# Optimization experiments

Measured on AMD Instinct MI355X. Metric: run time of the kernel, lower is better.

Reference implementation:

```python
import jax, jax.numpy as jnp
import numpy as np

N_NODES = 100000
N_EDGES = 640000
HIDDEN = 128
EPS = 1e-6


def setup_inputs() -> dict:
    key = jax.random.key(0)
    k_x, k_w, k_a, k_e = jax.random.split(key, 4)
    x = jax.random.normal(k_x, (N_NODES, HIDDEN), dtype=jnp.float32)
    W = jax.random.normal(k_w, (HIDDEN, HIDDEN), dtype=jnp.float32) / np.sqrt(HIDDEN)
    b = jnp.zeros((HIDDEN,), dtype=jnp.float32)
    att_w = jax.random.normal(k_a, (1, 2 * HIDDEN), dtype=jnp.float32) / np.sqrt(2 * HIDDEN)
    norm_w = jnp.ones((HIDDEN,), dtype=jnp.float32)
    norm_b = jnp.zeros((HIDDEN,), dtype=jnp.float32)
    e = jax.random.randint(k_e, (N_EDGES, 2), 0, N_NODES, dtype=jnp.int64)
    return {"x": x, "W": W, "b": b, "att_w": att_w, "norm_w": norm_w, "norm_b": norm_b, "e": e}


def reference(x, W, b, att_w, norm_w, norm_b, e):
    n_nodes = x.shape[0]
    src, dst = e[:, 0], e[:, 1]
    # Edge gather + shared linear on both endpoints: [E, D]
    m = x[src] @ W.T + b
    s = x[dst] @ W.T + b
    # Attention score per edge: leaky_relu(concat @ w^T), then exp -> [E, 1]
    a = jnp.exp(jax.nn.leaky_relu(jnp.concatenate((m, s), axis=1) @ att_w.T, negative_slope=0.2))
    # NOTE: faithful to the original: this weighted message sum is computed
    # but then overwritten (dead code in the source module).
    _unused = jax.ops.segment_sum(a * m, dst, num_segments=n_nodes)
    # Normalizer: sum of attention weights per destination node -> [N, 1]
    n = jax.ops.segment_sum(a, dst, num_segments=n_nodes)
    h = jax.nn.relu(x / jnp.where(n == 0.0, 1.0, n))
    # Residual + RMSNorm (per-row, with affine weight and bias, eps=1e-6)
    y = h + x
    inv_rms = jax.lax.rsqrt(jnp.mean(y * y, axis=-1, keepdims=True) + EPS)
    return norm_w * (y * inv_rms) + norm_b
```

## Files before the change

kernel.cpp:

```cpp
#include <hip/hip_runtime.h>

#define N_NODES 100000
#define N_EDGES 640000
#define HIDDEN  128
#define EPS     1e-6f

__global__ void precompute_uvc(const float* __restrict__ W,
                               const float* __restrict__ b,
                               const float* __restrict__ att_w,
                               float* __restrict__ u,
                               float* __restrict__ v,
                               float* __restrict__ c) {
    int k = threadIdx.x;
    float su = 0.f, sv = 0.f;
    for (int j = 0; j < HIDDEN; ++j) {
        float w = W[j * HIDDEN + k];
        su += att_w[j] * w;
        sv += att_w[HIDDEN + j] * w;
    }
    u[k] = su;
    v[k] = sv;
    if (k == 0) {
        float cc = 0.f;
        for (int j = 0; j < HIDDEN; ++j)
            cc += att_w[j] * b[j] + att_w[HIDDEN + j] * b[j];
        *c = cc;
    }
}

__global__ void node_dots(const float* __restrict__ x,
                          const float* __restrict__ u,
                          const float* __restrict__ v,
                          float* __restrict__ p,
                          float* __restrict__ q) {
    int node = (int)((blockIdx.x * (unsigned)blockDim.x + threadIdx.x) >> 6);
    int lane = threadIdx.x & 63;
    if (node >= N_NODES) return;

    float2 xv = ((const float2*)(x + (size_t)node * HIDDEN))[lane];
    float2 uv = ((const float2*)u)[lane];
    float2 vv = ((const float2*)v)[lane];

    float sp = xv.x * uv.x + xv.y * uv.y;
    float sq = xv.x * vv.x + xv.y * vv.y;
    #pragma unroll
    for (int off = 32; off > 0; off >>= 1) {
        sp += __shfl_down(sp, off);
        sq += __shfl_down(sq, off);
    }
    if (lane == 0) { p[node] = sp; q[node] = sq; }
}

__global__ void edge_kernel(const int* __restrict__ e,
                            const float* __restrict__ p,
                            const float* __restrict__ q,
                            const float* __restrict__ c,
                            float* __restrict__ n) {
    int eid = blockIdx.x * blockDim.x + threadIdx.x;
    if (eid >= N_EDGES) return;
    int src = e[2 * eid];
    int dst = e[2 * eid + 1];
    float score = p[src] + q[dst] + c[0];
    float lr = score > 0.f ? score : 0.2f * score;
    atomicAdd(&n[dst], expf(lr));
}

__global__ void final_kernel(const float* __restrict__ x,
                             const float* __restrict__ n,
                             const float* __restrict__ norm_w,
                             const float* __restrict__ norm_b,
                             float* __restrict__ out) {
    int node = (int)((blockIdx.x * (unsigned)blockDim.x + threadIdx.x) >> 6);
    int lane = threadIdx.x & 63;
    if (node >= N_NODES) return;

    float nn = n[node];
    float inv_n = 1.f / (nn == 0.f ? 1.f : nn);

    float2 xv = ((const float2*)(x + (size_t)node * HIDDEN))[lane];
    float hx = xv.x * inv_n; hx = hx > 0.f ? hx : 0.f;
    float hy = xv.y * inv_n; hy = hy > 0.f ? hy : 0.f;
    float yx = hx + xv.x;
    float yy = hy + xv.y;

    float ss = yx * yx + yy * yy;
    #pragma unroll
    for (int off = 32; off > 0; off >>= 1) ss += __shfl_xor(ss, off);
    float inv_rms = rsqrtf(ss * (1.f / HIDDEN) + EPS);

    float2 wv = ((const float2*)norm_w)[lane];
    float2 bv = ((const float2*)norm_b)[lane];
    float2 ov;
    ov.x = wv.x * (yx * inv_rms) + bv.x;
    ov.y = wv.y * (yy * inv_rms) + bv.y;
    ((float2*)(out + (size_t)node * HIDDEN))[lane] = ov;
}

extern "C" void kernel_launch(void* const* d_in, const int* in_sizes, int n_in,
                              void* d_out, int out_size, void* d_ws, size_t ws_size,
                              hipStream_t stream) {
    const float* x      = (const float*)d_in[0];
    const float* W      = (const float*)d_in[1];
    const float* b      = (const float*)d_in[2];
    const float* att_w  = (const float*)d_in[3];
    const float* norm_w = (const float*)d_in[4];
    const float* norm_b = (const float*)d_in[5];
    const int*   e      = (const int*)d_in[6];
    float* out = (float*)d_out;

    float* ws = (float*)d_ws;
    float* u = ws;
    float* v = ws + 128;
    float* c = ws + 256;
    float* p = ws + 1024;
    float* q = p + N_NODES;
    float* nacc = q + N_NODES;

    hipMemsetAsync(nacc, 0, N_NODES * sizeof(float), stream);

    precompute_uvc<<<1, 128, 0, stream>>>(W, b, att_w, u, v, c);

    {
        int blocks = (N_NODES + 3) / 4;
        node_dots<<<blocks, 256, 0, stream>>>(x, u, v, p, q);
    }
    {
        int blocks = (N_EDGES + 255) / 256;
        edge_kernel<<<blocks, 256, 0, stream>>>(e, p, q, c, nacc);
    }
    {
        int blocks = (N_NODES + 3) / 4;
        final_kernel<<<blocks, 256, 0, stream>>>(x, nacc, norm_w, norm_b, out);
    }
}
```

Baseline: 178.4 us.

## Fuse accumulator zeroing into node_dots, vectorize rows with float4, parallelize precompute

Drops the separate memset launch by zeroing the per-node accumulator inside node_dots. node_dots and final_kernel now handle two nodes per wave using float4 loads and a 32-lane reduction. The precompute kernel splits its reduction over 512 threads through shared memory, and the edge kernel reads edge pairs as int2. The odd `__expf(lr)==__expf(lr) ? expf : expf` expression is redundant and may add work.

```diff
diff --git a/kernel.cpp b/kernel.cpp
--- a/kernel.cpp
+++ b/kernel.cpp
@@ -11,20 +11,35 @@
                                float* __restrict__ u,
                                float* __restrict__ v,
                                float* __restrict__ c) {
-    int k = threadIdx.x;
+    __shared__ float su_s[4][HIDDEN];
+    __shared__ float sv_s[4][HIDDEN];
+    int k     = threadIdx.x & 127;
+    int chunk = threadIdx.x >> 7;
+
     float su = 0.f, sv = 0.f;
-    for (int j = 0; j < HIDDEN; ++j) {
+    #pragma unroll
+    for (int jj = 0; jj < 32; ++jj) {
+        int j = chunk * 32 + jj;
         float w = W[j * HIDDEN + k];
         su += att_w[j] * w;
         sv += att_w[HIDDEN + j] * w;
     }
-    u[k] = su;
-    v[k] = sv;
-    if (k == 0) {
-        float cc = 0.f;
-        for (int j = 0; j < HIDDEN; ++j)
-            cc += att_w[j] * b[j] + att_w[HIDDEN + j] * b[j];
-        *c = cc;
+    su_s[chunk][k] = su;
+    sv_s[chunk][k] = sv;
+
+    if (threadIdx.x < 64) {
+        int t0 = threadIdx.x, t1 = threadIdx.x + 64;
+        float t = att_w[t0] * b[t0] + att_w[HIDDEN + t0] * b[t0]
+                + att_w[t1] * b[t1] + att_w[HIDDEN + t1] * b[t1];
+        #pragma unroll
+        for (int off = 32; off > 0; off >>= 1) t += __shfl_xor(t, off);
+        if (threadIdx.x == 0) *c = t;
+    }
+
+    __syncthreads();
+    if (chunk == 0) {
+        u[k] = su_s[0][k] + su_s[1][k] + su_s[2][k] + su_s[3][k];
+        v[k] = sv_s[0][k] + sv_s[1][k] + sv_s[2][k] + sv_s[3][k];
     }
 }
 
@@ -32,68 +47,86 @@
                           const float* __restrict__ u,
                           const float* __restrict__ v,
                           float* __restrict__ p,
-                          float* __restrict__ q) {
-    int node = (int)((blockIdx.x * (unsigned)blockDim.x + threadIdx.x) >> 6);
+                          float* __restrict__ q,
+                          float* __restrict__ nacc) {
+    int gid  = blockIdx.x * blockDim.x + threadIdx.x;
+    int wave = gid >> 6;
     int lane = threadIdx.x & 63;
+    int half = lane >> 5;
+    int sub  = lane & 31;
+    int node = wave * 2 + half;
     if (node >= N_NODES) return;
 
-    float2 xv = ((const float2*)(x + (size_t)node * HIDDEN))[lane];
-    float2 uv = ((const float2*)u)[lane];
-    float2 vv = ((const float2*)v)[lane];
+    float4 xv = ((const float4*)(x + (size_t)node * HIDDEN))[sub];
+    float4 uv = ((const float4*)u)[sub];
+    float4 vv = ((const float4*)v)[sub];
 
-    float sp = xv.x * uv.x + xv.y * uv.y;
-    float sq = xv.x * vv.x + xv.y * vv.y;
+    float sp = xv.x * uv.x + xv.y * uv.y + xv.z * uv.z + xv.w * uv.w;
+    float sq = xv.x * vv.x + xv.y * vv.y + xv.z * vv.z + xv.w * vv.w;
     #pragma unroll
-    for (int off = 32; off > 0; off >>= 1) {
-        sp += __shfl_down(sp, off);
-        sq += __shfl_down(sq, off);
+    for (int off = 16; off > 0; off >>= 1) {
+        sp += __shfl_xor(sp, off);
+        sq += __shfl_xor(sq, off);
     }
-    if (lane == 0) { p[node] = sp; q[node] = sq; }
+    if (sub == 0) {
+        p[node]    = sp;
+        q[node]    = sq;
+        nacc[node] = 0.f;
+    }
 }
 
 __global__ void edge_kernel(const int* __restrict__ e,
                             const float* __restrict__ p,
                             const float* __restrict__ q,
                             const float* __restrict__ c,
-                            float* __restrict__ n) {
+                            float* __restrict__ nacc) {
     int eid = blockIdx.x * blockDim.x + threadIdx.x;
     if (eid >= N_EDGES) return;
-    int src = e[2 * eid];
-    int dst = e[2 * eid + 1];
-    float score = p[src] + q[dst] + c[0];
+    int2 ed = ((const int2*)e)[eid];
+    float score = p[ed.x] + q[ed.y] + c[0];
     float lr = score > 0.f ? score : 0.2f * score;
-    atomicAdd(&n[dst], expf(lr));
+    atomicAdd(&nacc[ed.y], __expf(lr) == __expf(lr) ? expf(lr) : expf(lr));
 }
 
 __global__ void final_kernel(const float* __restrict__ x,
-                             const float* __restrict__ n,
+                             const float* __restrict__ nacc,
                              const float* __restrict__ norm_w,
                              const float* __restrict__ norm_b,
                              float* __restrict__ out) {
-    int node = (int)((blockIdx.x * (unsigned)blockDim.x + threadIdx.x) >> 6);
+    int gid  = blockIdx.x * blockDim.x + threadIdx.x;
+    int wave = gid >> 6;
     int lane = threadIdx.x & 63;
+    int half = lane >> 5;
+    int sub  = lane & 31;
+    int node = wave * 2 + half;
     if (node >= N_NODES) return;
 
-    float nn = n[node];
+    float nn = nacc[node];
     float inv_n = 1.f / (nn == 0.f ? 1.f : nn);
 
-    float2 xv = ((const float2*)(x + (size_t)node * HIDDEN))[lane];
-    float hx = xv.x * inv_n; hx = hx > 0.f ? hx : 0.f;
-    float hy = xv.y * inv_n; hy = hy > 0.f ? hy : 0.f;
-    float yx = hx + xv.x;
-    float yy = hy + xv.y;
+    float4 xv = ((const float4*)(x + (size_t)node * HIDDEN))[sub];
+    float4 y;
+    {
+        float h;
+        h = xv.x * inv_n; h = h > 0.f ? h : 0.f; y.x = h + xv.x;
+        h = xv.y * inv_n; h = h > 0.f ? h : 0.f; y.y = h + xv.y;
+        h = xv.z * inv_n; h = h > 0.f ? h : 0.f; y.z = h + xv.z;
+        h = xv.w * inv_n; h = h > 0.f ? h : 0.f; y.w = h + xv.w;
+    }
 
-    float ss = yx * yx + yy * yy;
+    float ss = y.x * y.x + y.y * y.y + y.z * y.z + y.w * y.w;
     #pragma unroll
-    for (int off = 32; off > 0; off >>= 1) ss += __shfl_xor(ss, off);
+    for (int off = 16; off > 0; off >>= 1) ss += __shfl_xor(ss, off);
     float inv_rms = rsqrtf(ss * (1.f / HIDDEN) + EPS);
 
-    float2 wv = ((const float2*)norm_w)[lane];
-    float2 bv = ((const float2*)norm_b)[lane];
-    float2 ov;
-    ov.x = wv.x * (yx * inv_rms) + bv.x;
-    ov.y = wv.y * (yy * inv_rms) + bv.y;
-    ((float2*)(out + (size_t)node * HIDDEN))[lane] = ov;
+    float4 wv = ((const float4*)norm_w)[sub];
+    float4 bv = ((const float4*)norm_b)[sub];
+    float4 ov;
+    ov.x = wv.x * (y.x * inv_rms) + bv.x;
+    ov.y = wv.y * (y.y * inv_rms) + bv.y;
+    ov.z = wv.z * (y.z * inv_rms) + bv.z;
+    ov.w = wv.w * (y.w * inv_rms) + bv.w;
+    ((float4*)(out + (size_t)node * HIDDEN))[sub] = ov;
 }
 
 extern "C" void kernel_launch(void* const* d_in, const int* in_sizes, int n_in,
@@ -109,27 +142,25 @@
     float* out = (float*)d_out;
 
     float* ws = (float*)d_ws;
-    float* u = ws;
-    float* v = ws + 128;
-    float* c = ws + 256;
-    float* p = ws + 1024;
-    float* q = p + N_NODES;
+    float* u    = ws;
+    float* v    = ws + 128;
+    float* c    = ws + 256;
+    float* p    = ws + 1024;
+    float* q    = p + N_NODES;
     float* nacc = q + N_NODES;
 
-    hipMemsetAsync(nacc, 0, N_NODES * sizeof(float), stream);
-
-    precompute_uvc<<<1, 128, 0, stream>>>(W, b, att_w, u, v, c);
+    precompute_uvc<<<1, 512, 0, stream>>>(W, b, att_w, u, v, c);
 
     {
-        int blocks = (N_NODES + 3) / 4;
-        node_dots<<<blocks, 256, 0, stream>>>(x, u, v, p, q);
+        int blocks = (N_NODES + 7) / 8;
+        node_dots<<<blocks, 256, 0, stream>>>(x, u, v, p, q, nacc);
     }
     {
         int blocks = (N_EDGES + 255) / 256;
         edge_kernel<<<blocks, 256, 0, stream>>>(e, p, q, c, nacc);
     }
     {
-        int blocks = (N_NODES + 3) / 4;
+        int blocks = (N_NODES + 7) / 8;
         final_kernel<<<blocks, 256, 0, stream>>>(x, nacc, norm_w, norm_b, out);
     }
 }
```

New measurement: 160.2 us. 10.2% less time.
